# Kernel optimization log

Hardware: AMD Instinct MI355X
Metric: run time of the kernel (lower is better)

## Reference

```python
import jax, jax.numpy as jnp
import numpy as np

B, S, D = 2, 1024, 4096
N_HEADS, KV_HEADS, HEAD_DIM = 32, 8, 128
EPS = 1e-6
ROPE_THETA = 1e6


def setup_inputs() -> dict:
    key = jax.random.key(0)
    ks = jax.random.split(key, 7)
    scale = 0.02
    x = jax.random.normal(ks[0], (B, S, D), dtype=jnp.float32)
    positions = jnp.broadcast_to(jnp.arange(S, dtype=jnp.int32)[None, :], (B, S))
    wq = jax.random.normal(ks[1], (D, N_HEADS, HEAD_DIM), dtype=jnp.float32) * scale
    wk = jax.random.normal(ks[2], (D, KV_HEADS, HEAD_DIM), dtype=jnp.float32) * scale
    wv = jax.random.normal(ks[3], (D, KV_HEADS, HEAD_DIM), dtype=jnp.float32) * scale
    wo = jax.random.normal(ks[4], (N_HEADS, HEAD_DIM, D), dtype=jnp.float32) * scale
    q_norm_w = 1.0 + jax.random.normal(ks[5], (HEAD_DIM,), dtype=jnp.float32) * 0.01
    k_norm_w = 1.0 + jax.random.normal(ks[6], (HEAD_DIM,), dtype=jnp.float32) * 0.01
    return {"x": x, "positions": positions, "wq": wq, "wk": wk, "wv": wv,
            "wo": wo, "q_norm_w": q_norm_w, "k_norm_w": k_norm_w}


def _rms_norm(t, w):
    # per-head RMSNorm over last (head_dim) axis
    var = jnp.mean(jnp.square(t), axis=-1, keepdims=True)
    return (t * jax.lax.rsqrt(var + EPS)) * w


def _rope(t, positions):
    # neox-style rotary embedding; t: [B, S, n, H], positions: [B, S]
    half = t.shape[-1] // 2
    inv_freq = 1.0 / (ROPE_THETA ** (jnp.arange(0, half, dtype=jnp.float32) / half))
    ang = positions.astype(jnp.float32)[..., None] * inv_freq  # [B, S, half]
    cos = jnp.cos(ang)[:, :, None, :]  # [B, S, 1, half]
    sin = jnp.sin(ang)[:, :, None, :]
    t1, t2 = t[..., :half], t[..., half:]
    return jnp.concatenate([t1 * cos - t2 * sin, t2 * cos + t1 * sin], axis=-1)


def reference(x, positions, wq, wk, wv, wo, q_norm_w, k_norm_w):
    # QKV projections (einsum layers: 'bsd,dnh->bsnh')
    q = jnp.einsum('bsd,dnh->bsnh', x, wq)  # [B, S, N, H]
    k = jnp.einsum('bsd,dkh->bskh', x, wk)  # [B, S, K, H]
    v = jnp.einsum('bsd,dkh->bskh', x, wv)
    # per-head QK RMSNorm, then RoPE
    q = _rope(_rms_norm(q, q_norm_w), positions)
    k = _rope(_rms_norm(k, k_norm_w), positions)
    # GQA: expand KV heads to query heads
    groups = N_HEADS // KV_HEADS
    k = jnp.repeat(k, groups, axis=2)  # [B, S, N, H]
    v = jnp.repeat(v, groups, axis=2)
    sm_scale = HEAD_DIM ** -0.5
    scores = jnp.einsum('bqnh,btnh->bnqt', q, k) * sm_scale  # [B, N, S, S]
    causal = jnp.tril(jnp.ones((S, S), dtype=bool))
    scores = jnp.where(causal[None, None], scores, jnp.finfo(scores.dtype).min)
    probs = jax.nn.softmax(scores, axis=-1)
    attn = jnp.einsum('bnqt,btnh->bqnh', probs, v)  # [B, S, N, H]
    out = jnp.einsum('bqnh,nhd->bqd', attn, wo)  # output projection
    return out
```

## Files before the change

kernel.cpp:

```cpp
#include <hip/hip_runtime.h>
#include <stdint.h>

#define S_LEN   1024
#define D_MODEL 4096
#define NHQ     32
#define NKV     8
#define HD      128
#define NTOK    2048
#define NQKV    6144
#define SM_SCALE 0.08838834764831843f

typedef __attribute__((ext_vector_type(8))) __bf16 bf16x8;
typedef __attribute__((ext_vector_type(4))) float f32x4;

__device__ __forceinline__ unsigned short f2bf(float f) {
  union { float f; unsigned u; } x; x.f = f;
  unsigned r = x.u + 0x7fffu + ((x.u >> 16) & 1u);
  return (unsigned short)(r >> 16);
}

__device__ __forceinline__ void gload_lds16(const void* g, void* l) {
  __builtin_amdgcn_global_load_lds((__attribute__((address_space(1))) void*)g,
                                   (__attribute__((address_space(3))) void*)l,
                                   16, 0, 0);
}

__global__ void k_f32_to_bf16(const float* __restrict__ in,
                              unsigned short* __restrict__ out, int n8) {
  int i = blockIdx.x * blockDim.x + threadIdx.x;
  if (i >= n8) return;
  const float4* p = (const float4*)(in + (size_t)i * 8);
  float4 v0 = p[0], v1 = p[1];
  uint4 o;
  o.x = f2bf(v0.x) | ((unsigned)f2bf(v0.y) << 16);
  o.y = f2bf(v0.z) | ((unsigned)f2bf(v0.w) << 16);
  o.z = f2bf(v1.x) | ((unsigned)f2bf(v1.y) << 16);
  o.w = f2bf(v1.z) | ((unsigned)f2bf(v1.w) << 16);
  *(uint4*)(out + (size_t)i * 8) = o;
}

__global__ void k_transpose(const float* __restrict__ in,
                            unsigned short* __restrict__ out, int R, int C) {
  __shared__ float t[32][33];
  int c = threadIdx.x & 31, r0 = threadIdx.x >> 5;
  int cb = blockIdx.x * 32, rb = blockIdx.y * 32;
#pragma unroll
  for (int i = 0; i < 4; ++i) {
    int r = r0 + i * 8;
    t[r][c] = in[(size_t)(rb + r) * C + cb + c];
  }
  __syncthreads();
#pragma unroll
  for (int i = 0; i < 4; ++i) {
    int r = r0 + i * 8;
    out[(size_t)(cb + r) * R + rb + c] = f2bf(t[c][r]);
  }
}


#define STG(Gptr, rowbase, ksrc, half, bufi, matoff)                            \
  { int kcl = (ksrc) < NT ? (ksrc) : NT - 1;                                    \
    _Pragma("unroll")                                                           \
    for (int i_ = 0; i_ < 2; ++i_) {                                            \
      int lin = i_ * 512 + tid;                                                 \
      int r_ = lin >> 2, slot = lin & 3;                                        \
      int sw = slot ^ ((r_ >> 1) & 3);                                          \
      gload_lds16(Gptr + (size_t)((rowbase) + r_) * K + kcl * 64 + (half) * 32 + sw * 8, \
                  smem + (bufi) * 65536 + (matoff) + (half) * 16384 + lin * 16); \
    } }

#define PHASE(mh, kstep, STAGE_STMT, DO_VMCNT)                                  \
  {                                                                             \
    const char* Ab = smem + cur * 65536 + (kstep) * 16384;                      \
    const char* Bb = smem + cur * 65536 + 32768 + (kstep) * 16384;              \
    bf16x8 af[4], bfr[4];                                                       \
    _Pragma("unroll")                                                           \
    for (int mf = 0; mf < 4; ++mf) {                                            \
      int row = wr * 128 + (mh) * 64 + mf * 16 + lr;                            \
      af[mf] = *(const bf16x8*)(Ab + row * 64 + ((lg * 16) ^ (((row >> 1) & 3) << 4))); \
    }                                                                           \
    _Pragma("unroll")                                                           \
    for (int nf = 0; nf < 4; ++nf) {                                            \
      int row = wc * 64 + nf * 16 + lr;                                         \
      bfr[nf] = *(const bf16x8*)(Bb + row * 64 + ((lg * 16) ^ (((row >> 1) & 3) << 4))); \
    }                                                                           \
    STAGE_STMT;                                                                 \
    if (DO_VMCNT) asm volatile("s_waitcnt vmcnt(6)" ::: "memory");              \
    __builtin_amdgcn_s_barrier();                                               \
    asm volatile("s_waitcnt lgkmcnt(0)" ::: "memory");                          \
    __builtin_amdgcn_sched_barrier(0);                                          \
    __builtin_amdgcn_s_setprio(1);                                              \
    _Pragma("unroll")                                                           \
    for (int mf = 0; mf < 4; ++mf)                                              \
      _Pragma("unroll")                                                         \
      for (int nf = 0; nf < 4; ++nf)                                            \
        acc[(mh) * 4 + mf][nf] =                                                \
            __builtin_amdgcn_mfma_f32_16x16x32_bf16(af[mf], bfr[nf], acc[(mh) * 4 + mf][nf], 0, 0, 0); \
    __builtin_amdgcn_s_setprio(0);                                              \
    __builtin_amdgcn_s_barrier();                                               \
  }

__global__ __launch_bounds__(512, 2) void k_gemm256(
    const unsigned short* __restrict__ A,
    const unsigned short* __restrict__ Bt,
    float* __restrict__ C, int M, int N, int K, int ldc, int nbx) {
  extern __shared__ __align__(16) char smem[];
  int tid = threadIdx.x;
  int l = tid & 63;
  int w = tid >> 6;
  int lr = l & 15, lg = l >> 4;
  int wr = w >> 2, wc = w & 3;
  int nwg = gridDim.x;
  int q8 = nwg >> 3;
  int o = blockIdx.x;
  int wg = (o & 7) * q8 + (o >> 3);
  int by = wg / nbx, bx = wg - by * nbx;
  int bm = by * 256, bn = bx * 256;
  int NT = K >> 6;

  f32x4 acc[8][4] = {};

  STG(A, bm, 0, 0, 0, 0); STG(Bt, bn, 0, 0, 0, 32768);
  STG(A, bm, 0, 1, 0, 0); STG(Bt, bn, 0, 1, 0, 32768);
  STG(A, bm, 1, 0, 1, 0); STG(Bt, bn, 1, 0, 1, 32768);
  asm volatile("s_waitcnt vmcnt(8)" ::: "memory");
  __builtin_amdgcn_s_barrier();

  for (int kt = 0; kt < NT; ++kt) {
    int cur = kt & 1;
    PHASE(0, 0, STG(A, bm, kt + 1, 1, cur ^ 1, 0), 0)
    PHASE(1, 0, STG(Bt, bn, kt + 1, 1, cur ^ 1, 32768), 1)
    PHASE(0, 1, STG(A, bm, kt + 2, 0, cur, 0), 0)
    PHASE(1, 1, STG(Bt, bn, kt + 2, 0, cur, 32768), 1)
  }

#pragma unroll
  for (int mh = 0; mh < 2; ++mh)
#pragma unroll
    for (int mf = 0; mf < 4; ++mf)
#pragma unroll
      for (int nf = 0; nf < 4; ++nf)
#pragma unroll
        for (int j = 0; j < 4; ++j)
          C[(size_t)(bm + wr * 128 + mh * 64 + mf * 16 + lg * 4 + j) * ldc +
            bn + wc * 64 + nf * 16 + lr] = acc[mh * 4 + mf][nf][j];
}

__global__ void k_norm_rope(const float* __restrict__ qkv, const float* __restrict__ w,
                            const int* __restrict__ positions,
                            unsigned short* __restrict__ out, int nheads, int colbase,
                            float oscale) {
  int wid = blockIdx.x * 4 + (threadIdx.x >> 6);
  int lane = threadIdx.x & 63;
  int token = wid / nheads, head = wid - token * nheads;
  const float* src = qkv + (size_t)token * NQKV + colbase + head * HD;
  float e0 = src[lane], e1 = src[lane + 64];
  float ss = e0 * e0 + e1 * e1;
#pragma unroll
  for (int m = 1; m < 64; m <<= 1) ss += __shfl_xor(ss, m, 64);
  float rs = rsqrtf(ss * (1.0f / 128.0f) + 1e-6f);
  float n0 = e0 * rs * w[lane], n1 = e1 * rs * w[lane + 64];
  int pos = positions[token];
  float invf = exp2f((float)lane * (-19.931568569324174f / 64.0f));
  float ang = (float)pos * invf;
  float sv, cv;
  sincosf(ang, &sv, &cv);
  float o0 = (n0 * cv - n1 * sv) * oscale;
  float o1 = (n1 * cv + n0 * sv) * oscale;
  int b = token >> 10, s = token & 1023;
  size_t ob = ((size_t)(b * nheads + head) * S_LEN + s) * HD;
  out[ob + lane] = f2bf(o0);
  out[ob + 64 + lane] = f2bf(o1);
}

__global__ void k_v_transpose(const float* __restrict__ qkv, unsigned short* __restrict__ vt) {
  __shared__ float t[32][33];
  int slice = blockIdx.z;
  int b = slice >> 3, kh = slice & 7;
  const float* in = qkv + (size_t)(b * S_LEN) * NQKV + 5120 + kh * HD;
  unsigned short* out = vt + (size_t)slice * HD * S_LEN;
  int c = threadIdx.x & 31, r0 = threadIdx.x >> 5;
  int s0 = blockIdx.y * 32, d0 = blockIdx.x * 32;
#pragma unroll
  for (int i = 0; i < 4; ++i) {
    int r = r0 + i * 8;
    t[r][c] = in[(size_t)(s0 + r) * NQKV + d0 + c];
  }
  __syncthreads();
#pragma unroll
  for (int i = 0; i < 4; ++i) {
    int r = r0 + i * 8;
    out[(size_t)(d0 + r) * S_LEN + s0 + c] = f2bf(t[c][r]);
  }
}

__global__ __launch_bounds__(256) void k_attn(const unsigned short* __restrict__ qh,
                                              const unsigned short* __restrict__ kbuf,
                                              const unsigned short* __restrict__ vtbuf,
                                              unsigned short* __restrict__ attn_out) {
  __shared__ __align__(16) unsigned short k_lds[64 * 128];
  __shared__ __align__(16) unsigned short v_lds[128 * 64];
  __shared__ __align__(16) unsigned short p_lds[4][16 * 64];
  int b = blockIdx.z, h = blockIdx.y, bx = blockIdx.x;
  int khd = h >> 2;
  int tid = threadIdx.x, w = tid >> 6, l = tid & 63;
  int lr = l & 15, lg = l >> 4;
  const unsigned short* K = kbuf + (size_t)(b * NKV + khd) * S_LEN * HD;
  const unsigned short* VT = vtbuf + (size_t)(b * NKV + khd) * HD * S_LEN;
  char* klp = (char*)k_lds;
  char* vlp = (char*)v_lds;
  char* plp = (char*)p_lds[w];
  int swz = (lr & 7) << 4;

  for (int strip = 0; strip < 2; ++strip) {
    int qs = strip ? (15 - bx) : bx;
    int q0 = qs * 64;
    const unsigned short* Q = qh + ((size_t)(b * NHQ + h) * S_LEN + q0 + w * 16) * HD;
    bf16x8 qf[4];
#pragma unroll
    for (int kk = 0; kk < 4; ++kk)
      qf[kk] = *(const bf16x8*)&Q[(size_t)lr * HD + kk * 32 + lg * 8];

    f32x4 o[8] = {};
    float m_[4], l_[4];
#pragma unroll
    for (int j = 0; j < 4; ++j) { m_[j] = -1e30f; l_[j] = 0.0f; }

    int nt = qs + 1;
    for (int t = 0; t < nt; ++t) {
      int t0 = t * 64;
      __syncthreads();
#pragma unroll
      for (int it = 0; it < 4; ++it) {
        int db = (tid + it * 256) * 16;
        int kr = db >> 8, kc = db & 255;
        gload_lds16(K + (size_t)(t0 + kr) * HD + ((kc ^ ((kr & 7) << 4)) >> 1), klp + db);
        int vr = db >> 7, vc = db & 127;
        gload_lds16(VT + (size_t)vr * S_LEN + t0 + ((vc ^ ((vr & 7) << 4)) >> 1), vlp + db);
      }
      __syncthreads();

      f32x4 sc[4];
      __builtin_amdgcn_s_setprio(1);
#pragma unroll
      for (int ct = 0; ct < 4; ++ct) {
        f32x4 s = {};
        int row = ct * 16 + lr;
#pragma unroll
        for (int kk = 0; kk < 4; ++kk) {
          bf16x8 kf = *(const bf16x8*)(klp + row * 256 + ((kk * 64 + lg * 16) ^ swz));
          s = __builtin_amdgcn_mfma_f32_16x16x32_bf16(qf[kk], kf, s, 0, 0, 0);
        }
        sc[ct] = s;
      }
      __builtin_amdgcn_s_setprio(0);

      bool full = (t < qs);
      float alpha[4];
#pragma unroll
      for (int j = 0; j < 4; ++j) {
        if (!full) {
          int rg = q0 + w * 16 + lg * 4 + j;
#pragma unroll
          for (int ct = 0; ct < 4; ++ct)
            sc[ct][j] = (t0 + ct * 16 + lr <= rg) ? sc[ct][j] : -1e30f;
        }
        float mx = fmaxf(fmaxf(sc[0][j], sc[1][j]), fmaxf(sc[2][j], sc[3][j]));
#pragma unroll
        for (int msk = 1; msk < 16; msk <<= 1) mx = fmaxf(mx, __shfl_xor(mx, msk, 64));
        float mn = fmaxf(m_[j], mx);
        alpha[j] = __expf(m_[j] - mn);
        int q = lg * 4 + j;
        int psw = (q & 7) << 4;
        float ps = 0.0f;
#pragma unroll
        for (int ct = 0; ct < 4; ++ct) {
          float p = __expf(sc[ct][j] - mn);
          ps += p;
          *(unsigned short*)(plp + q * 128 + (((ct * 16 + lr) * 2) ^ psw)) = f2bf(p);
        }
#pragma unroll
        for (int msk = 1; msk < 16; msk <<= 1) ps += __shfl_xor(ps, msk, 64);
        l_[j] = l_[j] * alpha[j] + ps;
        m_[j] = mn;
      }
#pragma unroll
      for (int dc = 0; dc < 8; ++dc) {
        o[dc][0] *= alpha[0]; o[dc][1] *= alpha[1];
        o[dc][2] *= alpha[2]; o[dc][3] *= alpha[3];
      }
      asm volatile("s_waitcnt lgkmcnt(0)" ::: "memory");
      __builtin_amdgcn_s_setprio(1);
#pragma unroll
      for (int kt = 0; kt < 2; ++kt) {
        bf16x8 pa = *(const bf16x8*)(plp + lr * 128 + ((kt * 64 + lg * 16) ^ swz));
#pragma unroll
        for (int dc = 0; dc < 8; ++dc) {
          int vrow = dc * 16 + lr;
          bf16x8 vf = *(const bf16x8*)(vlp + vrow * 128 + ((kt * 64 + lg * 16) ^ swz));
          o[dc] = __builtin_amdgcn_mfma_f32_16x16x32_bf16(pa, vf, o[dc], 0, 0, 0);
        }
      }
      __builtin_amdgcn_s_setprio(0);
    }

#pragma unroll
    for (int j = 0; j < 4; ++j) {
      int rg = q0 + w * 16 + lg * 4 + j;
      size_t row = (size_t)(b * S_LEN + rg) * D_MODEL + h * HD;
      float inv = 1.0f / l_[j];
#pragma unroll
      for (int dc = 0; dc < 8; ++dc)
        attn_out[row + dc * 16 + lr] = f2bf(o[dc][j] * inv);
    }
  }
}

extern "C" void kernel_launch(void* const* d_in, const int* in_sizes, int n_in,
                              void* d_out, int out_size, void* d_ws, size_t ws_size,
                              hipStream_t stream) {
  const float* x        = (const float*)d_in[0];
  const int* positions  = (const int*)d_in[1];
  const float* wq       = (const float*)d_in[2];
  const float* wk       = (const float*)d_in[3];
  const float* wv       = (const float*)d_in[4];
  const float* wo       = (const float*)d_in[5];
  const float* qnw      = (const float*)d_in[6];
  const float* knw      = (const float*)d_in[7];
  float* out            = (float*)d_out;

  char* ws = (char*)d_ws;
  unsigned short* xb   = (unsigned short*)(ws);
  unsigned short* wB   = (unsigned short*)(ws + 16777216);
  unsigned short* woT  = (unsigned short*)(ws + 67108864);
  float*          qkv  = (float*)(ws + 100663296);
  unsigned short* qh   = wB;
  unsigned short* khb  = (unsigned short*)(ws + 33554432);
  unsigned short* vtb  = (unsigned short*)(ws + 37748736);
  unsigned short* attn = xb;

  dim3 tb(256);
  k_f32_to_bf16<<<4096, tb, 0, stream>>>(x, xb, 1048576);
  k_transpose<<<dim3(128, 128), tb, 0, stream>>>(wq, wB, 4096, 4096);
  k_transpose<<<dim3(32, 128), tb, 0, stream>>>(wk, wB + (size_t)4096 * 4096, 4096, 1024);
  k_transpose<<<dim3(32, 128), tb, 0, stream>>>(wv, wB + (size_t)5120 * 4096, 4096, 1024);
  k_transpose<<<dim3(128, 128), tb, 0, stream>>>(wo, woT, 4096, 4096);

  k_gemm256<<<dim3(192), dim3(512), 131072, stream>>>(xb, wB, qkv, 2048, 6144, 4096, 6144, 24);

  k_norm_rope<<<16384, tb, 0, stream>>>(qkv, qnw, positions, qh, 32, 0, SM_SCALE);
  k_norm_rope<<<4096, tb, 0, stream>>>(qkv, knw, positions, khb, 8, 4096, 1.0f);
  k_v_transpose<<<dim3(4, 32, 16), tb, 0, stream>>>(qkv, vtb);

  k_attn<<<dim3(8, 32, 2), tb, 0, stream>>>(qh, khb, vtb, attn);

  k_gemm256<<<dim3(128), dim3(512), 131072, stream>>>(attn, woT, out, 2048, 4096, 4096, 4096, 16);
}
```

Baseline: 364.9 us.

## Prefetch LDS fragments ahead of MFMA and split-K the output projection GEMM

```diff
diff --git a/kernel.cpp b/kernel.cpp
--- a/kernel.cpp
+++ b/kernel.cpp
@@ -65,45 +65,51 @@
       int lin = i_ * 512 + tid;                                                 \
       int r_ = lin >> 2, slot = lin & 3;                                        \
       int sw = slot ^ ((r_ >> 1) & 3);                                          \
-      gload_lds16(Gptr + (size_t)((rowbase) + r_) * K + kcl * 64 + (half) * 32 + sw * 8, \
+      gload_lds16(Gptr + (size_t)((rowbase) + r_) * Kstride + k0e + kcl * 64 + (half) * 32 + sw * 8, \
                   smem + (bufi) * 65536 + (matoff) + (half) * 16384 + lin * 16); \
     } }
 
-#define PHASE(mh, kstep, STAGE_STMT, DO_VMCNT)                                  \
-  {                                                                             \
-    const char* Ab = smem + cur * 65536 + (kstep) * 16384;                      \
-    const char* Bb = smem + cur * 65536 + 32768 + (kstep) * 16384;              \
-    bf16x8 af[4], bfr[4];                                                       \
+#define RD_AF(dst, mh, ks, bufi)                                                \
+  _Pragma("unroll")                                                             \
+  for (int mf = 0; mf < 4; ++mf) {                                              \
+    int row = wr * 128 + (mh) * 64 + mf * 16 + lr;                              \
+    dst[mf] = *(const bf16x8*)(smem + (bufi) * 65536 + (ks) * 16384 + row * 64  \
+                               + ((lg * 16) ^ (((row >> 1) & 3) << 4)));        \
+  }
+
+#define RD_BF(dst, ks, bufi)                                                    \
+  _Pragma("unroll")                                                             \
+  for (int nf = 0; nf < 4; ++nf) {                                              \
+    int row = wc * 64 + nf * 16 + lr;                                           \
+    dst[nf] = *(const bf16x8*)(smem + (bufi) * 65536 + 32768 + (ks) * 16384 + row * 64 \
+                               + ((lg * 16) ^ (((row >> 1) & 3) << 4)));        \
+  }
+
+#define MFMA16(mh, AF, BF)                                                      \
+  __builtin_amdgcn_s_setprio(1);                                                \
+  _Pragma("unroll")                                                             \
+  for (int mf = 0; mf < 4; ++mf)                                                \
     _Pragma("unroll")                                                           \
-    for (int mf = 0; mf < 4; ++mf) {                                            \
-      int row = wr * 128 + (mh) * 64 + mf * 16 + lr;                            \
-      af[mf] = *(const bf16x8*)(Ab + row * 64 + ((lg * 16) ^ (((row >> 1) & 3) << 4))); \
-    }                                                                           \
-    _Pragma("unroll")                                                           \
-    for (int nf = 0; nf < 4; ++nf) {                                            \
-      int row = wc * 64 + nf * 16 + lr;                                         \
-      bfr[nf] = *(const bf16x8*)(Bb + row * 64 + ((lg * 16) ^ (((row >> 1) & 3) << 4))); \
-    }                                                                           \
-    STAGE_STMT;                                                                 \
-    if (DO_VMCNT) asm volatile("s_waitcnt vmcnt(6)" ::: "memory");              \
-    __builtin_amdgcn_s_barrier();                                               \
-    asm volatile("s_waitcnt lgkmcnt(0)" ::: "memory");                          \
-    __builtin_amdgcn_sched_barrier(0);                                          \
-    __builtin_amdgcn_s_setprio(1);                                              \
-    _Pragma("unroll")                                                           \
-    for (int mf = 0; mf < 4; ++mf)                                              \
-      _Pragma("unroll")                                                         \
-      for (int nf = 0; nf < 4; ++nf)                                            \
-        acc[(mh) * 4 + mf][nf] =                                                \
-            __builtin_amdgcn_mfma_f32_16x16x32_bf16(af[mf], bfr[nf], acc[(mh) * 4 + mf][nf], 0, 0, 0); \
-    __builtin_amdgcn_s_setprio(0);                                              \
-    __builtin_amdgcn_s_barrier();                                               \
-  }
+    for (int nf = 0; nf < 4; ++nf)                                              \
+      acc[(mh) * 4 + mf][nf] = __builtin_amdgcn_mfma_f32_16x16x32_bf16(         \
+          AF[mf], BF[nf], acc[(mh) * 4 + mf][nf], 0, 0, 0);                     \
+  __builtin_amdgcn_s_setprio(0);
+
+#define PHASE(STG_STMT, RD_STMT, MFMA_STMT)                                     \
+  asm volatile("s_waitcnt lgkmcnt(0)" ::: "memory");                            \
+  __builtin_amdgcn_sched_barrier(0);                                            \
+  STG_STMT;                                                                     \
+  asm volatile("s_waitcnt vmcnt(6)" ::: "memory");                              \
+  RD_STMT;                                                                      \
+  __builtin_amdgcn_sched_barrier(0);                                            \
+  MFMA_STMT;                                                                    \
+  __builtin_amdgcn_s_barrier();
 
 __global__ __launch_bounds__(512, 2) void k_gemm256(
     const unsigned short* __restrict__ A,
     const unsigned short* __restrict__ Bt,
-    float* __restrict__ C, int M, int N, int K, int ldc, int nbx) {
+    float* __restrict__ C, int Kstride, int ldc, int nbx, int ksplit, int NT,
+    int use_atomic) {
   extern __shared__ __align__(16) char smem[];
   int tid = threadIdx.x;
   int l = tid & 63;
@@ -114,24 +120,37 @@
   int q8 = nwg >> 3;
   int o = blockIdx.x;
   int wg = (o & 7) * q8 + (o >> 3);
-  int by = wg / nbx, bx = wg - by * nbx;
+  int tiles = nwg / ksplit;
+  int ks = wg / tiles;
+  int wgt = wg - ks * tiles;
+  int by = wgt / nbx, bx = wgt - by * nbx;
   int bm = by * 256, bn = bx * 256;
-  int NT = K >> 6;
+  int k0e = ks * NT * 64;
 
   f32x4 acc[8][4] = {};
+  bf16x8 af0[4], af1[4], bf0[4], bf1[4];
 
   STG(A, bm, 0, 0, 0, 0); STG(Bt, bn, 0, 0, 0, 32768);
   STG(A, bm, 0, 1, 0, 0); STG(Bt, bn, 0, 1, 0, 32768);
   STG(A, bm, 1, 0, 1, 0); STG(Bt, bn, 1, 0, 1, 32768);
   asm volatile("s_waitcnt vmcnt(8)" ::: "memory");
   __builtin_amdgcn_s_barrier();
+  RD_AF(af0, 0, 0, 0) RD_BF(bf0, 0, 0)
 
   for (int kt = 0; kt < NT; ++kt) {
     int cur = kt & 1;
-    PHASE(0, 0, STG(A, bm, kt + 1, 1, cur ^ 1, 0), 0)
-    PHASE(1, 0, STG(Bt, bn, kt + 1, 1, cur ^ 1, 32768), 1)
-    PHASE(0, 1, STG(A, bm, kt + 2, 0, cur, 0), 0)
-    PHASE(1, 1, STG(Bt, bn, kt + 2, 0, cur, 32768), 1)
+    PHASE(STG(A, bm, kt + 1, 1, cur ^ 1, 0),
+          { RD_AF(af1, 1, 0, cur) },
+          MFMA16(0, af0, bf0))
+    PHASE(STG(Bt, bn, kt + 1, 1, cur ^ 1, 32768),
+          { RD_AF(af0, 0, 1, cur) RD_BF(bf1, 1, cur) },
+          MFMA16(1, af1, bf0))
+    PHASE(STG(A, bm, kt + 2, 0, cur, 0),
+          { RD_AF(af1, 1, 1, cur) },
+          MFMA16(0, af0, bf1))
+    PHASE(STG(Bt, bn, kt + 2, 0, cur, 32768),
+          { RD_AF(af0, 0, 0, cur ^ 1) RD_BF(bf0, 0, cur ^ 1) },
+          MFMA16(1, af1, bf1))
   }
 
 #pragma unroll
@@ -141,9 +160,13 @@
 #pragma unroll
       for (int nf = 0; nf < 4; ++nf)
 #pragma unroll
-        for (int j = 0; j < 4; ++j)
-          C[(size_t)(bm + wr * 128 + mh * 64 + mf * 16 + lg * 4 + j) * ldc +
-            bn + wc * 64 + nf * 16 + lr] = acc[mh * 4 + mf][nf][j];
+        for (int j = 0; j < 4; ++j) {
+          size_t idx = (size_t)(bm + wr * 128 + mh * 64 + mf * 16 + lg * 4 + j) * ldc +
+                       bn + wc * 64 + nf * 16 + lr;
+          float v = acc[mh * 4 + mf][nf][j];
+          if (use_atomic) atomicAdd(&C[idx], v);
+          else C[idx] = v;
+        }
 }
 
 __global__ void k_norm_rope(const float* __restrict__ qkv, const float* __restrict__ w,
@@ -340,13 +363,15 @@
   unsigned short* attn = xb;
 
   dim3 tb(256);
+  hipMemsetAsync(out, 0, (size_t)out_size * 4, stream);
+
   k_f32_to_bf16<<<4096, tb, 0, stream>>>(x, xb, 1048576);
   k_transpose<<<dim3(128, 128), tb, 0, stream>>>(wq, wB, 4096, 4096);
   k_transpose<<<dim3(32, 128), tb, 0, stream>>>(wk, wB + (size_t)4096 * 4096, 4096, 1024);
   k_transpose<<<dim3(32, 128), tb, 0, stream>>>(wv, wB + (size_t)5120 * 4096, 4096, 1024);
   k_transpose<<<dim3(128, 128), tb, 0, stream>>>(wo, woT, 4096, 4096);
 
-  k_gemm256<<<dim3(192), dim3(512), 131072, stream>>>(xb, wB, qkv, 2048, 6144, 4096, 6144, 24);
+  k_gemm256<<<dim3(192), dim3(512), 131072, stream>>>(xb, wB, qkv, 4096, 6144, 24, 1, 64, 0);
 
   k_norm_rope<<<16384, tb, 0, stream>>>(qkv, qnw, positions, qh, 32, 0, SM_SCALE);
   k_norm_rope<<<4096, tb, 0, stream>>>(qkv, knw, positions, khb, 8, 4096, 1.0f);
@@ -354,5 +379,5 @@
 
   k_attn<<<dim3(8, 32, 2), tb, 0, stream>>>(qh, khb, vtb, attn);
 
-  k_gemm256<<<dim3(128), dim3(512), 131072, stream>>>(attn, woT, out, 2048, 4096, 4096, 4096, 16);
-}
+  k_gemm256<<<dim3(256), dim3(512), 131072, stream>>>(attn, woT, out, 4096, 4096, 16, 2, 32, 1);
+}
```

After: 372.5 us. 2.1% more time.
